# Kernel optimization log

Hardware: AMD Instinct MI355X
Metric: run time of the kernel (lower is better)

## Reference

```python
import jax, jax.numpy as jnp
import numpy as np

N = 8192        # nodes
E = 262144      # edges (avg degree 32)
D = 128         # input_dim
H = 128         # hidden_dim
O = 64          # output_dim (classes)
C = 4096        # codebook_size
LAMB_EDGE = 1.0
LAMB_NODE = 1.0
COMMIT_W = 0.25


def l2norm(x):
    return x / jnp.clip(jnp.linalg.norm(x, axis=-1, keepdims=True), 1e-12)


def graph_conv(x, W, b, src, dst, n):
    # DGL GraphConv, norm='both': D_out^{-1/2} on src, sum-aggregate, D_in^{-1/2} on dst, then xW+b, relu
    ones = jnp.ones(src.shape[0], x.dtype)
    deg_out = jax.ops.segment_sum(ones, src, num_segments=n)
    deg_in = jax.ops.segment_sum(ones, dst, num_segments=n)
    norm_src = jnp.where(deg_out > 0, jax.lax.rsqrt(jnp.maximum(deg_out, 1e-12)), 0.0)
    norm_dst = jnp.where(deg_in > 0, jax.lax.rsqrt(jnp.maximum(deg_in, 1e-12)), 0.0)
    h = x * norm_src[:, None]
    m = jax.ops.segment_sum(h[src], dst, num_segments=n)  # message passing (irregular gather/scatter)
    h = m * norm_dst[:, None]
    return jax.nn.relu(h @ W + b)


def setup_inputs() -> dict:
    key = jax.random.key(0)
    ks = jax.random.split(key, 16)
    feats = jax.random.normal(ks[0], (N, D), jnp.float32)
    src = jax.random.randint(ks[1], (E,), 0, N)
    dst = jax.random.randint(ks[2], (E,), 0, N)
    s = 1.0 / np.sqrt(D)
    sh = 1.0 / np.sqrt(H)
    return {
        'feats': feats, 'src': src, 'dst': dst,
        'W1': jax.random.normal(ks[3], (D, D), jnp.float32) * s,
        'b1': jnp.zeros((D,), jnp.float32),
        'W2': jax.random.normal(ks[4], (D, H), jnp.float32) * s,
        'b2': jnp.zeros((H,), jnp.float32),
        'dec1_W': jax.random.normal(ks[5], (D, D), jnp.float32) * s,
        'dec1_b': jnp.zeros((D,), jnp.float32),
        'dec2_W': jax.random.normal(ks[6], (D, D), jnp.float32) * s,
        'dec2_b': jnp.zeros((D,), jnp.float32),
        'lin_W': jax.random.normal(ks[7], (H, O), jnp.float32) * sh,
        'lin_b': jnp.zeros((O,), jnp.float32),
        'codebook': jax.random.normal(ks[8], (C, D), jnp.float32),
    }


def reference(feats, src, dst, W1, b1, W2, b2, dec1_W, dec1_b, dec2_W, dec2_b, lin_W, lin_b, codebook):
    n = feats.shape[0]
    # layer 1: GraphConv(D -> D)
    h1 = graph_conv(feats, W1, b1, src, dst, n)  # [N, D]

    # VectorQuantize with cosine similarity codebook
    xn = l2norm(h1)
    cn = l2norm(codebook)                 # [C, D]
    dist = xn @ cn.T                      # [N, C] cosine similarity
    ind = jnp.argmax(dist, axis=-1)       # [N]
    q = cn[ind]                           # [N, D] nearest (normalized) codes
    commit_loss = COMMIT_W * jnp.mean((jax.lax.stop_gradient(q) - h1) ** 2)
    quantized = h1 + jax.lax.stop_gradient(q - h1)  # straight-through

    quantized_edge = quantized @ dec1_W + dec1_b
    quantized_node = quantized @ dec2_W + dec2_b
    feature_rec_loss = LAMB_NODE * jnp.mean((h1 - quantized_node) ** 2)

    # dense adjacency reconstruction
    adj = jnp.zeros((n, n), feats.dtype).at[src, dst].set(1.0)
    adj_q = quantized_edge @ quantized_edge.T          # [N, N]
    adj_q = (adj_q - adj_q.min()) / (adj_q.max() - adj_q.min())
    edge_rec_loss = LAMB_EDGE * jnp.sqrt(jnp.mean((adj - adj_q) ** 2))

    # layer 2: GraphConv(D -> H) on quantized_edge, then linear head
    h3 = graph_conv(quantized_edge, W2, b2, src, dst, n)
    out = h3 @ lin_W + lin_b                           # [N, O]

    loss = feature_rec_loss + edge_rec_loss + commit_loss
    h_list = (h1, quantized, h3)
    return (h_list, out, loss, dist, cn)
```

## Files before the change

kernel.cpp:

```cpp
#include <hip/hip_runtime.h>
#include <cstdint>

constexpr int N = 8192, E = 262144, D = 128, O = 64, C = 4096;

#define DEV __device__ __forceinline__

typedef short s8v __attribute__((ext_vector_type(8)));
typedef float f4v __attribute__((ext_vector_type(4)));

DEV unsigned fmap(float f) {
  unsigned u = __float_as_uint(f);
  return (u & 0x80000000u) ? ~u : (u | 0x80000000u);
}
DEV float funmap(unsigned u) {
  unsigned o = (u & 0x80000000u) ? (u & 0x7FFFFFFFu) : ~u;
  return __uint_as_float(o);
}
DEV unsigned short f2bf(float f) {
  uint32_t b = __float_as_uint(f);
  return (unsigned short)((b + 0x7FFFu + ((b >> 16) & 1u)) >> 16);
}
DEV float bf2f(unsigned short h) { return __uint_as_float((uint32_t)h << 16); }


__global__ __launch_bounds__(256) void k_degree(const int* __restrict__ src, const int* __restrict__ dst,
    uint32_t* __restrict__ bits, int* __restrict__ dego, int* __restrict__ degi,
    uint32_t* __restrict__ scal_u) {
  int e = blockIdx.x * 256 + threadIdx.x;
  int s = src[e], d = dst[e];
  atomicAdd(&dego[s], 1);
  atomicAdd(&degi[d], 1);
  unsigned idx = (unsigned)s * 8192u + (unsigned)d;
  unsigned bit = 1u << (idx & 31);
  unsigned old = atomicOr(&bits[idx >> 5], bit);
  bool isnew = !(old & bit);
  unsigned long long b = __ballot(isnew);
  if ((threadIdx.x & 63) == 0) atomicAdd(&scal_u[2], (unsigned)__popcll(b));
}

__global__ __launch_bounds__(256) void k_norms(const int* __restrict__ dego, const int* __restrict__ degi,
                                               float* __restrict__ nsrc, float* __restrict__ ndst) {
  int i = blockIdx.x * 256 + threadIdx.x;
  if (i >= N) return;
  int a = dego[i], b = degi[i];
  nsrc[i] = a > 0 ? 1.0f / sqrtf((float)a) : 0.0f;
  ndst[i] = b > 0 ? 1.0f / sqrtf((float)b) : 0.0f;
}

__global__ __launch_bounds__(1024) void k_scan(const int* __restrict__ degi, int* __restrict__ rowptr,
                                               int* __restrict__ cursor) {
  __shared__ int sh[1024];
  int tid = threadIdx.x;
  int base = tid * 8;
  int v[8];
  int s = 0;
#pragma unroll
  for (int j = 0; j < 8; ++j) { v[j] = degi[base + j]; s += v[j]; }
  sh[tid] = s;
  __syncthreads();
  for (int off = 1; off < 1024; off <<= 1) {
    int t = (tid >= off) ? sh[tid - off] : 0;
    __syncthreads();
    sh[tid] += t;
    __syncthreads();
  }
  int run = (tid == 0) ? 0 : sh[tid - 1];
#pragma unroll
  for (int j = 0; j < 8; ++j) { rowptr[base + j] = run; cursor[base + j] = run; run += v[j]; }
  if (tid == 1023) rowptr[N] = run;
}

__global__ __launch_bounds__(256) void k_scatter(const int* __restrict__ src, const int* __restrict__ dst,
                                                 int* __restrict__ cursor, int* __restrict__ csr) {
  int e = blockIdx.x * 256 + threadIdx.x;
  int d = dst[e];
  int pos = atomicAdd(&cursor[d], 1);
  csr[pos] = src[e];
}

__global__ __launch_bounds__(256) void k_scale(const float4* __restrict__ in, const float* __restrict__ norm,
                                               float4* __restrict__ out) {
  int i = blockIdx.x * 256 + threadIdx.x;
  if (i >= N * 32) return;
  float s = norm[i >> 5];
  float4 v = in[i];
  v.x *= s; v.y *= s; v.z *= s; v.w *= s;
  out[i] = v;
}

__global__ __launch_bounds__(256) void k_tobf16(const float4* __restrict__ in, ushort4* __restrict__ out) {
  int i = blockIdx.x * 256 + threadIdx.x;
  if (i >= N * 32) return;
  float4 v = in[i];
  ushort4 o;
  o.x = f2bf(v.x); o.y = f2bf(v.y); o.z = f2bf(v.z); o.w = f2bf(v.w);
  out[i] = o;
}

__global__ __launch_bounds__(256) void k_split(const float4* __restrict__ in,
    ushort4* __restrict__ hi, ushort4* __restrict__ lo, int n4) {
  int i = blockIdx.x * 256 + threadIdx.x;
  if (i >= n4) return;
  float4 v = in[i];
  ushort4 h, l;
  h.x = f2bf(v.x); h.y = f2bf(v.y); h.z = f2bf(v.z); h.w = f2bf(v.w);
  l.x = f2bf(v.x - bf2f(h.x)); l.y = f2bf(v.y - bf2f(h.y));
  l.z = f2bf(v.z - bf2f(h.z)); l.w = f2bf(v.w - bf2f(h.w));
  hi[i] = h; lo[i] = l;
}

__global__ __launch_bounds__(128) void k_aggregate(const int* __restrict__ rowptr, const int* __restrict__ csr,
    const float* __restrict__ tmp, const float* __restrict__ ndst, float* __restrict__ out) {
  int row = blockIdx.x, t = threadIdx.x;
  int e0 = rowptr[row], e1 = rowptr[row + 1];
  float acc = 0.f;
  int e = e0;
  for (; e + 4 <= e1; e += 4) {
    int s0 = csr[e], s1 = csr[e + 1], s2 = csr[e + 2], s3 = csr[e + 3];
    acc += tmp[s0 * 128 + t];
    acc += tmp[s1 * 128 + t];
    acc += tmp[s2 * 128 + t];
    acc += tmp[s3 * 128 + t];
  }
  for (; e < e1; ++e) acc += tmp[csr[e] * 128 + t];
  out[row * 128 + t] = acc * ndst[row];
}

__global__ __launch_bounds__(256) void k_l2norm(const float* __restrict__ in, float* __restrict__ out_al,
                                                float* __restrict__ out_extra, int rows) {
  int wave = threadIdx.x >> 6, lane = threadIdx.x & 63;
  int row = blockIdx.x * 4 + wave;
  if (row >= rows) return;
  float2 v = ((const float2*)in)[row * 64 + lane];
  float ss = v.x * v.x + v.y * v.y;
#pragma unroll
  for (int o = 32; o > 0; o >>= 1) ss += __shfl_xor(ss, o);
  float den = fmaxf(sqrtf(ss), 1e-12f);
  float ox = v.x / den, oy = v.y / den;
  ((float2*)out_al)[row * 64 + lane] = make_float2(ox, oy);
  if (out_extra != nullptr) {
    out_extra[row * 128 + 2 * lane] = ox;
    out_extra[row * 128 + 2 * lane + 1] = oy;
  }
}

template <int CO, bool RELU>
__global__ __launch_bounds__(256, 2) void k_mm(const float* __restrict__ A, const float* __restrict__ W,
    const float* __restrict__ bias, float* __restrict__ out) {
  constexpr int CG = CO / 4;
  constexpr int RG = 256 / CG;
  constexpr int TR = RG * 4;
  constexpr int WIT = (64 * CG) / 256;
  __shared__ __align__(16) float Al[TR * 128];
  __shared__ __align__(16) float Wl[64 * CO];
  int tid = threadIdx.x;
  int cg = tid % CG, rg = tid / CG;
  int rbase = blockIdx.x * TR;
#pragma unroll
  for (int it = 0; it < TR / 8; ++it) {
    int idx = tid + it * 256;
    int r = idx >> 5, c = idx & 31;
    *(float4*)&Al[r * 128 + c * 4] = *(const float4*)&A[(rbase + r) * 128 + c * 4];
  }
  float acc[4][4] = {};
  for (int kc = 0; kc < 128; kc += 64) {
    __syncthreads();
#pragma unroll
    for (int it = 0; it < WIT; ++it) {
      int idx = tid + it * 256;
      int r = idx / CG, c = idx % CG;
      *(float4*)&Wl[r * CO + c * 4] = *(const float4*)&W[(kc + r) * CO + c * 4];
    }
    __syncthreads();
#pragma unroll
    for (int k = 0; k < 64; ++k) {
      float4 w4 = *(const float4*)&Wl[k * CO + cg * 4];
#pragma unroll
      for (int i = 0; i < 4; ++i) {
        float a = Al[(rg * 4 + i) * 128 + kc + k];
        acc[i][0] += a * w4.x; acc[i][1] += a * w4.y; acc[i][2] += a * w4.z; acc[i][3] += a * w4.w;
      }
    }
  }
  float4 b4 = *(const float4*)&bias[cg * 4];
#pragma unroll
  for (int i = 0; i < 4; ++i) {
    float4 o;
    o.x = acc[i][0] + b4.x; o.y = acc[i][1] + b4.y; o.z = acc[i][2] + b4.z; o.w = acc[i][3] + b4.w;
    if (RELU) { o.x = fmaxf(o.x, 0.f); o.y = fmaxf(o.y, 0.f); o.z = fmaxf(o.z, 0.f); o.w = fmaxf(o.w, 0.f); }
    *(float4*)&out[(rbase + rg * 4 + i) * CO + cg * 4] = o;
  }
}

__global__ __launch_bounds__(256) void k_dist(
    const unsigned short* __restrict__ xhi, const unsigned short* __restrict__ xlo,
    const unsigned short* __restrict__ chi, const unsigned short* __restrict__ clo,
    float* __restrict__ dout, unsigned long long* __restrict__ pbk, float* __restrict__ pbv2) {
  int bx = blockIdx.x, by = blockIdx.y;
  int rbase = by * 128, cbase = bx * 128;
  __shared__ __align__(16) unsigned short As[128 * 132];
  __shared__ __align__(16) unsigned short Bs[128 * 132];
  int tid = threadIdx.x;
  int wave = tid >> 6, lane = tid & 63;
  int l15 = lane & 15, quad = lane >> 4;
  int wr = wave * 32;

#pragma unroll
  for (int it = 0; it < 8; ++it) {
    int idx = tid + it * 256;
    int r = idx >> 4, ch = idx & 15;
    *(s8v*)&As[r * 132 + ch * 8] = *(const s8v*)&xhi[(rbase + r) * 128 + ch * 8];
    *(s8v*)&Bs[r * 132 + ch * 8] = *(const s8v*)&chi[(cbase + r) * 128 + ch * 8];
  }
  __syncthreads();
  s8v ah[2][4], al[2][4];
#pragma unroll
  for (int rt = 0; rt < 2; ++rt)
#pragma unroll
    for (int kq = 0; kq < 4; ++kq)
      ah[rt][kq] = *(const s8v*)&As[(wr + rt * 16 + l15) * 132 + kq * 32 + quad * 8];
  __syncthreads();
#pragma unroll
  for (int it = 0; it < 8; ++it) {
    int idx = tid + it * 256;
    int r = idx >> 4, ch = idx & 15;
    *(s8v*)&As[r * 132 + ch * 8] = *(const s8v*)&xlo[(rbase + r) * 128 + ch * 8];
  }
  __syncthreads();
#pragma unroll
  for (int rt = 0; rt < 2; ++rt)
#pragma unroll
    for (int kq = 0; kq < 4; ++kq)
      al[rt][kq] = *(const s8v*)&As[(wr + rt * 16 + l15) * 132 + kq * 32 + quad * 8];

  f4v acc[2][8];
#pragma unroll
  for (int rt = 0; rt < 2; ++rt)
#pragma unroll
    for (int ct = 0; ct < 8; ++ct) acc[rt][ct] = {0.f, 0.f, 0.f, 0.f};

#pragma unroll
  for (int ct = 0; ct < 8; ++ct) {
    s8v b[4];
#pragma unroll
    for (int kq = 0; kq < 4; ++kq)
      b[kq] = *(const s8v*)&Bs[(ct * 16 + l15) * 132 + kq * 32 + quad * 8];
#pragma unroll
    for (int rt = 0; rt < 2; ++rt)
#pragma unroll
      for (int kq = 0; kq < 4; ++kq) {
        acc[rt][ct] = __builtin_amdgcn_mfma_f32_16x16x32_bf16(ah[rt][kq], b[kq], acc[rt][ct], 0, 0, 0);
        acc[rt][ct] = __builtin_amdgcn_mfma_f32_16x16x32_bf16(al[rt][kq], b[kq], acc[rt][ct], 0, 0, 0);
      }
  }
  __syncthreads();
#pragma unroll
  for (int it = 0; it < 8; ++it) {
    int idx = tid + it * 256;
    int r = idx >> 4, ch = idx & 15;
    *(s8v*)&Bs[r * 132 + ch * 8] = *(const s8v*)&clo[(cbase + r) * 128 + ch * 8];
  }
  __syncthreads();
#pragma unroll
  for (int ct = 0; ct < 8; ++ct) {
    s8v b[4];
#pragma unroll
    for (int kq = 0; kq < 4; ++kq)
      b[kq] = *(const s8v*)&Bs[(ct * 16 + l15) * 132 + kq * 32 + quad * 8];
#pragma unroll
    for (int rt = 0; rt < 2; ++rt)
#pragma unroll
      for (int kq = 0; kq < 4; ++kq)
        acc[rt][ct] = __builtin_amdgcn_mfma_f32_16x16x32_bf16(ah[rt][kq], b[kq], acc[rt][ct], 0, 0, 0);
  }

  float b1v[2][4], b2v[2][4];
  unsigned c1v[2][4];
#pragma unroll
  for (int rt = 0; rt < 2; ++rt)
#pragma unroll
    for (int reg = 0; reg < 4; ++reg) { b1v[rt][reg] = -3.4e38f; b2v[rt][reg] = -3.4e38f; c1v[rt][reg] = 0; }
#pragma unroll
  for (int rt = 0; rt < 2; ++rt)
#pragma unroll
    for (int ct = 0; ct < 8; ++ct)
#pragma unroll
      for (int reg = 0; reg < 4; ++reg) {
        float v = acc[rt][ct][reg];
        int row = rbase + wr + rt * 16 + quad * 4 + reg;
        int col = cbase + ct * 16 + l15;
        dout[(size_t)row * 4096 + col] = v;
        if (v > b1v[rt][reg]) { b2v[rt][reg] = b1v[rt][reg]; b1v[rt][reg] = v; c1v[rt][reg] = (unsigned)col; }
        else if (v > b2v[rt][reg]) b2v[rt][reg] = v;
      }
  __syncthreads();
  unsigned long long* sck = (unsigned long long*)As;
  float* scv = (float*)Bs;
#pragma unroll
  for (int rt = 0; rt < 2; ++rt)
#pragma unroll
    for (int reg = 0; reg < 4; ++reg) {
      int rloc = wr + rt * 16 + quad * 4 + reg;
      sck[rloc * 16 + l15] =
          (((unsigned long long)fmap(b1v[rt][reg])) << 32) |
          (unsigned long long)(0xFFFFFFFFu - c1v[rt][reg]);
      scv[rloc * 16 + l15] = b2v[rt][reg];
    }
  __syncthreads();
  if (tid < 128) {
    unsigned long long m = 0ull;
#pragma unroll
    for (int l = 0; l < 16; ++l) {
      unsigned long long t = sck[tid * 16 + l];
      m = t > m ? t : m;
    }
    float v2 = -3.4e38f;
#pragma unroll
    for (int l = 0; l < 16; ++l) {
      unsigned long long k = sck[tid * 16 + l];
      float c = (k == m) ? scv[tid * 16 + l] : funmap((unsigned)(k >> 32));
      v2 = fmaxf(v2, c);
    }
    pbk[(size_t)(rbase + tid) * 32 + bx] = m;
    pbv2[(size_t)(rbase + tid) * 32 + bx] = v2;
  }
}

__global__ __launch_bounds__(128) void k_q(const unsigned long long* __restrict__ pbk,
    const float* __restrict__ pbv2, const float* __restrict__ xn, const float* __restrict__ cnws,
    const float* __restrict__ h1, float* __restrict__ qout, float* __restrict__ pq) {
  int row = blockIdx.x, t = threadIdx.x;
  int e = t & 31;
  unsigned long long k = pbk[(size_t)row * 32 + e];
  float v2l = pbv2[(size_t)row * 32 + e];
  unsigned long long m = k;
#pragma unroll
  for (int o = 32; o > 0; o >>= 1) {
    unsigned long long s = __shfl_xor(m, o);
    m = s > m ? s : m;
  }
  float cand = (k == m) ? v2l : funmap((unsigned)(k >> 32));
#pragma unroll
  for (int o = 32; o > 0; o >>= 1) cand = fmaxf(cand, __shfl_xor(cand, o));
  float gap = funmap((unsigned)(m >> 32)) - cand;
  int col;
  __shared__ float xr[128];
  __shared__ unsigned long long bw[2];
  if (gap < 2e-4f) {
    xr[t] = xn[row * 128 + t];
    __syncthreads();
    unsigned long long best = 0ull;
    for (int i = 0; i < 32; ++i) {
      int c = t + i * 128;
      const float* cp = &cnws[c * 128];
      float s = 0.f;
#pragma unroll 8
      for (int kk = 0; kk < 128; ++kk) s += xr[kk] * cp[kk];
      unsigned long long key = (((unsigned long long)fmap(s)) << 32) |
                               (unsigned long long)(0xFFFFFFFFu - (unsigned)c);
      if (key > best) best = key;
    }
#pragma unroll
    for (int o = 32; o > 0; o >>= 1) {
      unsigned long long s2 = __shfl_xor(best, o);
      best = s2 > best ? s2 : best;
    }
    if ((t & 63) == 0) bw[t >> 6] = best;
    __syncthreads();
    best = bw[0] > bw[1] ? bw[0] : bw[1];
    col = (int)(0xFFFFFFFFu - (unsigned)(best & 0xFFFFFFFFull));
  } else {
    col = (int)(0xFFFFFFFFu - (unsigned)(m & 0xFFFFFFFFull));
  }
  float q = cnws[col * 128 + t];
  qout[row * 128 + t] = q;
  float dd = q - h1[row * 128 + t];
  float ss = dd * dd;
#pragma unroll
  for (int o = 32; o > 0; o >>= 1) ss += __shfl_xor(ss, o);
  __shared__ float p[2];
  if ((t & 63) == 0) p[t >> 6] = ss;
  __syncthreads();
  if (t == 0) pq[row] = p[0] + p[1];
}

__global__ __launch_bounds__(256) void k_adjq(const unsigned short* __restrict__ qb,
    const uint32_t* __restrict__ bits,
    double* __restrict__ p_sum, double* __restrict__ p_sq, double* __restrict__ p_es,
    float* __restrict__ p_mn, float* __restrict__ p_mx) {
  int bx = blockIdx.x, by = blockIdx.y;
  int pid = by * gridDim.x + bx;
  int tid = threadIdx.x;
  if (bx < by) {
    if (tid == 0) {
      p_sum[pid] = 0.0; p_sq[pid] = 0.0; p_es[pid] = 0.0;
      p_mn[pid] = 3.4e38f; p_mx[pid] = -3.4e38f;
    }
    return;
  }
  int rbase = by * 128, cbase = bx * 128;
  __shared__ unsigned short Ab[128 * 132];
  __shared__ unsigned short Bb[128 * 132];
#pragma unroll
  for (int it = 0; it < 8; ++it) {
    int idx = tid + it * 256;
    int r = idx >> 4, ch = idx & 15;
    *(s8v*)&Ab[r * 132 + ch * 8] = *(const s8v*)&qb[(rbase + r) * 128 + ch * 8];
    *(s8v*)&Bb[r * 132 + ch * 8] = *(const s8v*)&qb[(cbase + r) * 128 + ch * 8];
  }
  __syncthreads();
  int wave = tid >> 6, lane = tid & 63;
  int l15 = lane & 15, quad = lane >> 4;
  int wr = wave * 32;
  f4v acc[2][8];
#pragma unroll
  for (int rt = 0; rt < 2; ++rt)
#pragma unroll
    for (int ct = 0; ct < 8; ++ct) acc[rt][ct] = {0.f, 0.f, 0.f, 0.f};
  s8v a[2][4];
#pragma unroll
  for (int rt = 0; rt < 2; ++rt)
#pragma unroll
    for (int kq = 0; kq < 4; ++kq)
      a[rt][kq] = *(const s8v*)&Ab[(wr + rt * 16 + l15) * 132 + kq * 32 + quad * 8];
#pragma unroll
  for (int ct = 0; ct < 8; ++ct) {
    s8v b[4];
#pragma unroll
    for (int kq = 0; kq < 4; ++kq)
      b[kq] = *(const s8v*)&Bb[(ct * 16 + l15) * 132 + kq * 32 + quad * 8];
#pragma unroll
    for (int rt = 0; rt < 2; ++rt)
#pragma unroll
      for (int kq = 0; kq < 4; ++kq)
        acc[rt][ct] = __builtin_amdgcn_mfma_f32_16x16x32_bf16(a[rt][kq], b[kq], acc[rt][ct], 0, 0, 0);
  }
  __syncthreads();
  uint32_t* bl = (uint32_t*)Ab;
  uint32_t* blT = bl + 512;
#pragma unroll
  for (int it = 0; it < 2; ++it) {
    int idx = tid + it * 256;
    int r = idx >> 2, wq = idx & 3;
    bl[idx] = bits[(rbase + r) * 256 + (cbase >> 5) + wq];
    blT[idx] = bits[(cbase + r) * 256 + (rbase >> 5) + wq];
  }
  __syncthreads();
  float lsum = 0.f, lsq = 0.f, les = 0.f;
  float lmin = 3.4e38f, lmax = -3.4e38f;
  bool diag = (bx == by);
#pragma unroll
  for (int rt = 0; rt < 2; ++rt)
#pragma unroll
    for (int ct = 0; ct < 8; ++ct)
#pragma unroll
      for (int reg = 0; reg < 4; ++reg) {
        int lr = wr + rt * 16 + quad * 4 + reg;
        int lc = ct * 16 + l15;
        if (diag && lc < lr) continue;
        float v = acc[rt][ct][reg];
        bool ondiag = diag && (lc == lr);
        float wgt = ondiag ? 1.f : 2.f;
        lsum += wgt * v;
        lsq += wgt * v * v;
        lmin = fminf(lmin, v);
        lmax = fmaxf(lmax, v);
        unsigned eb = (bl[lr * 4 + (lc >> 5)] >> (lc & 31)) & 1u;
        if (!ondiag) eb += (blT[lc * 4 + (lr >> 5)] >> (lr & 31)) & 1u;
        if (eb) les += (float)eb * v;
      }
  double dsum = (double)lsum, dsq = (double)lsq, des = (double)les;
#pragma unroll
  for (int o = 32; o > 0; o >>= 1) {
    dsum += __shfl_xor(dsum, o);
    dsq += __shfl_xor(dsq, o);
    des += __shfl_xor(des, o);
    lmin = fminf(lmin, __shfl_xor(lmin, o));
    lmax = fmaxf(lmax, __shfl_xor(lmax, o));
  }
  double* shd = (double*)Bb;
  float* shf = (float*)(shd + 12);
  if (lane == 0) {
    shd[wave * 3 + 0] = dsum; shd[wave * 3 + 1] = dsq; shd[wave * 3 + 2] = des;
    shf[wave * 2 + 0] = lmin; shf[wave * 2 + 1] = lmax;
  }
  __syncthreads();
  if (tid == 0) {
    double s = 0.0, q = 0.0, e = 0.0;
    float m0 = 3.4e38f, m1 = -3.4e38f;
#pragma unroll
    for (int w0 = 0; w0 < 4; ++w0) {
      s += shd[w0 * 3 + 0]; q += shd[w0 * 3 + 1]; e += shd[w0 * 3 + 2];
      m0 = fminf(m0, shf[w0 * 2 + 0]); m1 = fmaxf(m1, shf[w0 * 2 + 1]);
    }
    p_sum[pid] = s; p_sq[pid] = q; p_es[pid] = e;
    p_mn[pid] = m0; p_mx[pid] = m1;
  }
}

__global__ __launch_bounds__(256) void k_sqdiff(const float4* __restrict__ a, const float4* __restrict__ b,
                                                float* __restrict__ ps) {
  int i = blockIdx.x * 256 + threadIdx.x;
  float s = 0.f;
  const int total = N * 32;
  for (; i < total; i += gridDim.x * 256) {
    float4 x = a[i], y = b[i];
    float d0 = x.x - y.x, d1 = x.y - y.y, d2 = x.z - y.z, d3 = x.w - y.w;
    s += d0 * d0 + d1 * d1 + d2 * d2 + d3 * d3;
  }
#pragma unroll
  for (int o = 32; o > 0; o >>= 1) s += __shfl_xor(s, o);
  __shared__ float p[4];
  if ((threadIdx.x & 63) == 0) p[threadIdx.x >> 6] = s;
  __syncthreads();
  if (threadIdx.x == 0) ps[blockIdx.x] = p[0] + p[1] + p[2] + p[3];
}

__global__ __launch_bounds__(1024) void k_finish(const double* __restrict__ p_sum,
    const double* __restrict__ p_sq, const double* __restrict__ p_es,
    const float* __restrict__ p_mn, const float* __restrict__ p_mx,
    const float* __restrict__ pq, const float* __restrict__ ps,
    const uint32_t* __restrict__ scal_u, float* __restrict__ o_loss) {
  int tid = threadIdx.x;
  double sum = 0.0, sq = 0.0, es = 0.0, commit = 0.0, frec = 0.0;
  float mn = 3.4e38f, mx = -3.4e38f;
  for (int i = tid; i < 4096; i += 1024) {
    sum += p_sum[i]; sq += p_sq[i]; es += p_es[i];
    mn = fminf(mn, p_mn[i]); mx = fmaxf(mx, p_mx[i]);
  }
  for (int i = tid; i < 8192; i += 1024) commit += (double)pq[i];
  if (tid < 512) frec = (double)ps[tid];
#pragma unroll
  for (int o = 32; o > 0; o >>= 1) {
    sum += __shfl_xor(sum, o); sq += __shfl_xor(sq, o); es += __shfl_xor(es, o);
    commit += __shfl_xor(commit, o); frec += __shfl_xor(frec, o);
    mn = fminf(mn, __shfl_xor(mn, o)); mx = fmaxf(mx, __shfl_xor(mx, o));
  }
  __shared__ double shd[16][5];
  __shared__ float shf[16][2];
  int wave = tid >> 6, lane = tid & 63;
  if (lane == 0) {
    shd[wave][0] = sum; shd[wave][1] = sq; shd[wave][2] = es;
    shd[wave][3] = commit; shd[wave][4] = frec;
    shf[wave][0] = mn; shf[wave][1] = mx;
  }
  __syncthreads();
  if (tid == 0) {
    double s = 0, q = 0, e = 0, c = 0, f = 0;
    float m0 = 3.4e38f, m1 = -3.4e38f;
    for (int w0 = 0; w0 < 16; ++w0) {
      s += shd[w0][0]; q += shd[w0][1]; e += shd[w0][2]; c += shd[w0][3]; f += shd[w0][4];
      m0 = fminf(m0, shf[w0][0]); m1 = fmaxf(m1, shf[w0][1]);
    }
    double mnd = (double)m0, mxd = (double)m1, U = (double)scal_u[2];
    const double N2 = 67108864.0;
    double scl = 1.0 / (mxd - mnd);
    double mean = (scl * scl * (q - 2.0 * mnd * s + mnd * mnd * N2) - 2.0 * scl * (e - mnd * U) + U) / N2;
    *o_loss = (float)(f / 1048576.0 + sqrt(mean) + 0.25 * c / 1048576.0);
  }
}

extern "C" void kernel_launch(void* const* d_in, const int* in_sizes, int n_in,
                              void* d_out, int out_size, void* d_ws, size_t ws_size,
                              hipStream_t stream) {
  (void)in_sizes; (void)n_in; (void)out_size;
  const float* feats = (const float*)d_in[0];
  const int* src = (const int*)d_in[1];
  const int* dst = (const int*)d_in[2];
  const float* W1 = (const float*)d_in[3];
  const float* b1 = (const float*)d_in[4];
  const float* W2 = (const float*)d_in[5];
  const float* b2 = (const float*)d_in[6];
  const float* dec1W = (const float*)d_in[7];
  const float* dec1b = (const float*)d_in[8];
  const float* dec2W = (const float*)d_in[9];
  const float* dec2b = (const float*)d_in[10];
  const float* linW = (const float*)d_in[11];
  const float* linb = (const float*)d_in[12];
  const float* codebook = (const float*)d_in[13];

  float* out = (float*)d_out;
  float* o_h1 = out;
  float* o_q = out + 1048576;
  float* o_h3 = out + 2097152;
  float* o_out = out + 3145728;
  float* o_loss = out + 3670016;
  float* o_dist = out + 3670017;
  float* o_cn = out + 37224449;

  char* w = (char*)d_ws;
  size_t off = 0;
  auto alloc = [&](size_t b) { char* p = w + off; off = (off + b + 255) & ~(size_t)255; return p; };
  uint32_t* bits = (uint32_t*)alloc(8388608);
  int* dego = (int*)alloc(N * 4);
  int* degi = (int*)alloc(N * 4);
  uint32_t* scal_u = (uint32_t*)alloc(256);
  size_t zero_bytes = off;
  int* rowptr = (int*)alloc((N + 1) * 4);
  int* cursor = (int*)alloc(N * 4);
  int* csr = (int*)alloc(E * 4);
  float* nsrc = (float*)alloc(N * 4);
  float* ndst = (float*)alloc(N * 4);
  float* tmp = (float*)alloc((size_t)N * D * 4);
  float* agg = (float*)alloc((size_t)N * D * 4);
  float* xn = (float*)alloc((size_t)N * D * 4);
  float* cnws = (float*)alloc((size_t)C * D * 4);
  float* qe = (float*)alloc((size_t)N * D * 4);
  float* qn = (float*)alloc((size_t)N * D * 4);
  double* p_sum = (double*)alloc(4096 * 8);
  double* p_sq = (double*)alloc(4096 * 8);
  double* p_es = (double*)alloc(4096 * 8);
  float* p_mn = (float*)alloc(4096 * 4);
  float* p_mx = (float*)alloc(4096 * 4);
  float* pq = (float*)alloc(8192 * 4);
  float* ps = (float*)alloc(512 * 4);
  unsigned short* qb = (unsigned short*)tmp;
  unsigned short* xhi = (unsigned short*)qe;
  unsigned short* xlo = (unsigned short*)(qe + 524288);
  unsigned short* chi = (unsigned short*)qn;
  unsigned short* clo = (unsigned short*)(qn + 262144);
  unsigned long long* pbk = (unsigned long long*)agg;
  float* pbv2 = (float*)(agg + 524288);
  if (ws_size < off) return;

  hipMemsetAsync(d_ws, 0, zero_bytes, stream);

  k_degree<<<E / 256, 256, 0, stream>>>(src, dst, bits, dego, degi, scal_u);
  k_norms<<<N / 256, 256, 0, stream>>>(dego, degi, nsrc, ndst);
  k_scan<<<1, 1024, 0, stream>>>(degi, rowptr, cursor);
  k_scatter<<<E / 256, 256, 0, stream>>>(src, dst, cursor, csr);

  k_scale<<<N * 32 / 256, 256, 0, stream>>>((const float4*)feats, nsrc, (float4*)tmp);
  k_aggregate<<<N, 128, 0, stream>>>(rowptr, csr, tmp, ndst, agg);
  k_mm<128, true><<<N / 32, 256, 0, stream>>>(agg, W1, b1, o_h1);

  k_l2norm<<<C / 4, 256, 0, stream>>>(codebook, cnws, o_cn, C);
  k_l2norm<<<N / 4, 256, 0, stream>>>(o_h1, xn, nullptr, N);
  k_split<<<N * 32 / 256, 256, 0, stream>>>((const float4*)xn, (ushort4*)xhi, (ushort4*)xlo, N * 32);
  k_split<<<C * 32 / 256, 256, 0, stream>>>((const float4*)cnws, (ushort4*)chi, (ushort4*)clo, C * 32);
  k_dist<<<dim3(C / 128, N / 128), 256, 0, stream>>>(xhi, xlo, chi, clo, o_dist, pbk, pbv2);
  k_q<<<N, 128, 0, stream>>>(pbk, pbv2, xn, cnws, o_h1, o_q, pq);

  k_mm<128, false><<<N / 32, 256, 0, stream>>>(o_q, dec1W, dec1b, qe);
  k_mm<128, false><<<N / 32, 256, 0, stream>>>(o_q, dec2W, dec2b, qn);
  k_sqdiff<<<512, 256, 0, stream>>>((const float4*)o_h1, (const float4*)qn, ps);

  k_tobf16<<<N * 32 / 256, 256, 0, stream>>>((const float4*)qe, (ushort4*)qb);
  k_adjq<<<dim3(N / 128, N / 128), 256, 0, stream>>>(qb, bits, p_sum, p_sq, p_es, p_mn, p_mx);

  k_scale<<<N * 32 / 256, 256, 0, stream>>>((const float4*)qe, nsrc, (float4*)tmp);
  k_aggregate<<<N, 128, 0, stream>>>(rowptr, csr, tmp, ndst, agg);
  k_mm<128, true><<<N / 32, 256, 0, stream>>>(agg, W2, b2, o_h3);
  k_mm<64, false><<<N / 64, 256, 0, stream>>>(o_h3, linW, linb, o_out);

  k_finish<<<1, 1024, 0, stream>>>(p_sum, p_sq, p_es, p_mn, p_mx, pq, ps, scal_u, o_loss);
}
```

Baseline: 606.4 us.

## Defer near-tie argmax recomputation to a compacted fix-up kernel over a transposed codebook

The per-row quantize kernel no longer performs the exact fp32 rescan of all 4096 codes inside divergent blocks when the top-two gap is small. Instead it appends those rows to a flagged list through an atomic counter. A separate kernel then rescans only the flagged rows with 256 threads, reading a transposed codebook so the loads coalesce. This removes a long-tail stall from the N-block kernel, but adds a transpose kernel and an extra launch, and relies on scal_u[3] being zeroed by the memset.

```diff
diff --git a/kernel.cpp b/kernel.cpp
--- a/kernel.cpp
+++ b/kernel.cpp
@@ -109,6 +109,25 @@
   hi[i] = h; lo[i] = l;
 }
 
+__global__ __launch_bounds__(256) void k_transpose(const float* __restrict__ in, float* __restrict__ outT) {
+  __shared__ float tl[64][133];
+  int t = threadIdx.x;
+  int cbase = blockIdx.x * 64;
+#pragma unroll
+  for (int it = 0; it < 32; ++it) {
+    int idx = t + it * 256;
+    int r = idx >> 7, k = idx & 127;
+    tl[r][k] = in[(cbase + r) * 128 + k];
+  }
+  __syncthreads();
+#pragma unroll
+  for (int it = 0; it < 32; ++it) {
+    int idx = t + it * 256;
+    int k = idx >> 6, c = idx & 63;
+    outT[k * 4096 + cbase + c] = tl[c][k];
+  }
+}
+
 __global__ __launch_bounds__(128) void k_aggregate(const int* __restrict__ rowptr, const int* __restrict__ csr,
     const float* __restrict__ tmp, const float* __restrict__ ndst, float* __restrict__ out) {
   int row = blockIdx.x, t = threadIdx.x;
@@ -327,8 +346,9 @@
 }
 
 __global__ __launch_bounds__(128) void k_q(const unsigned long long* __restrict__ pbk,
-    const float* __restrict__ pbv2, const float* __restrict__ xn, const float* __restrict__ cnws,
-    const float* __restrict__ h1, float* __restrict__ qout, float* __restrict__ pq) {
+    const float* __restrict__ pbv2, const float* __restrict__ cnws,
+    const float* __restrict__ h1, float* __restrict__ qout, float* __restrict__ pq,
+    uint32_t* __restrict__ scal_u, int* __restrict__ flagged) {
   int row = blockIdx.x, t = threadIdx.x;
   int e = t & 31;
   unsigned long long k = pbk[(size_t)row * 32 + e];
@@ -343,35 +363,11 @@
 #pragma unroll
   for (int o = 32; o > 0; o >>= 1) cand = fmaxf(cand, __shfl_xor(cand, o));
   float gap = funmap((unsigned)(m >> 32)) - cand;
-  int col;
-  __shared__ float xr[128];
-  __shared__ unsigned long long bw[2];
-  if (gap < 2e-4f) {
-    xr[t] = xn[row * 128 + t];
-    __syncthreads();
-    unsigned long long best = 0ull;
-    for (int i = 0; i < 32; ++i) {
-      int c = t + i * 128;
-      const float* cp = &cnws[c * 128];
-      float s = 0.f;
-#pragma unroll 8
-      for (int kk = 0; kk < 128; ++kk) s += xr[kk] * cp[kk];
-      unsigned long long key = (((unsigned long long)fmap(s)) << 32) |
-                               (unsigned long long)(0xFFFFFFFFu - (unsigned)c);
-      if (key > best) best = key;
-    }
-#pragma unroll
-    for (int o = 32; o > 0; o >>= 1) {
-      unsigned long long s2 = __shfl_xor(best, o);
-      best = s2 > best ? s2 : best;
-    }
-    if ((t & 63) == 0) bw[t >> 6] = best;
-    __syncthreads();
-    best = bw[0] > bw[1] ? bw[0] : bw[1];
-    col = (int)(0xFFFFFFFFu - (unsigned)(best & 0xFFFFFFFFull));
-  } else {
-    col = (int)(0xFFFFFFFFu - (unsigned)(m & 0xFFFFFFFFull));
-  }
+  if (gap < 2e-4f && t == 0) {
+    unsigned idx = atomicAdd(&scal_u[3], 1u);
+    flagged[idx] = row;
+  }
+  int col = (int)(0xFFFFFFFFu - (unsigned)(m & 0xFFFFFFFFull));
   float q = cnws[col * 128 + t];
   qout[row * 128 + t] = q;
   float dd = q - h1[row * 128 + t];
@@ -382,6 +378,62 @@
   if ((t & 63) == 0) p[t >> 6] = ss;
   __syncthreads();
   if (t == 0) pq[row] = p[0] + p[1];
+}
+
+__global__ __launch_bounds__(256) void k_fix(const uint32_t* __restrict__ scal_u,
+    const int* __restrict__ flagged, const float* __restrict__ xn,
+    const float* __restrict__ cnwsT, const float* __restrict__ cnws,
+    const float* __restrict__ h1, float* __restrict__ qout, float* __restrict__ pq) {
+  int nf = (int)scal_u[3];
+  int t = threadIdx.x;
+  __shared__ float xr[128];
+  __shared__ unsigned long long bw4[4];
+  __shared__ float pp[2];
+  for (int i = blockIdx.x; i < nf; i += gridDim.x) {
+    int row = flagged[i];
+    __syncthreads();
+    if (t < 128) xr[t] = xn[row * 128 + t];
+    __syncthreads();
+    float s[16];
+#pragma unroll
+    for (int j = 0; j < 16; ++j) s[j] = 0.f;
+    for (int k = 0; k < 128; ++k) {
+      float xv = xr[k];
+      const float* cp = &cnwsT[k * 4096 + t];
+#pragma unroll
+      for (int j = 0; j < 16; ++j) s[j] = fmaf(xv, cp[j * 256], s[j]);
+    }
+    unsigned long long best = 0ull;
+#pragma unroll
+    for (int j = 0; j < 16; ++j) {
+      unsigned c = (unsigned)(j * 256 + t);
+      unsigned long long key = (((unsigned long long)fmap(s[j])) << 32) |
+                               (unsigned long long)(0xFFFFFFFFu - c);
+      if (key > best) best = key;
+    }
+#pragma unroll
+    for (int o = 32; o > 0; o >>= 1) {
+      unsigned long long s2 = __shfl_xor(best, o);
+      best = s2 > best ? s2 : best;
+    }
+    if ((t & 63) == 0) bw4[t >> 6] = best;
+    __syncthreads();
+    unsigned long long b0 = bw4[0] > bw4[1] ? bw4[0] : bw4[1];
+    unsigned long long b1 = bw4[2] > bw4[3] ? bw4[2] : bw4[3];
+    best = b0 > b1 ? b0 : b1;
+    int col = (int)(0xFFFFFFFFu - (unsigned)(best & 0xFFFFFFFFull));
+    if (t < 128) {
+      float q = cnws[col * 128 + t];
+      qout[(size_t)row * 128 + t] = q;
+      float dd = q - h1[row * 128 + t];
+      float ss = dd * dd;
+#pragma unroll
+      for (int o = 32; o > 0; o >>= 1) ss += __shfl_xor(ss, o);
+      if ((t & 63) == 0) pp[t >> 6] = ss;
+    }
+    __syncthreads();
+    if (t == 0) pq[row] = pp[0] + pp[1];
+  }
 }
 
 __global__ __launch_bounds__(256) void k_adjq(const unsigned short* __restrict__ qb,
@@ -614,7 +666,9 @@
   float* p_mx = (float*)alloc(4096 * 4);
   float* pq = (float*)alloc(8192 * 4);
   float* ps = (float*)alloc(512 * 4);
+  int* flagged = (int*)alloc(8192 * 4);
   unsigned short* qb = (unsigned short*)tmp;
+  float* cnwsT = tmp;
   unsigned short* xhi = (unsigned short*)qe;
   unsigned short* xlo = (unsigned short*)(qe + 524288);
   unsigned short* chi = (unsigned short*)qn;
@@ -636,10 +690,12 @@
 
   k_l2norm<<<C / 4, 256, 0, stream>>>(codebook, cnws, o_cn, C);
   k_l2norm<<<N / 4, 256, 0, stream>>>(o_h1, xn, nullptr, N);
+  k_transpose<<<C / 64, 256, 0, stream>>>(cnws, cnwsT);
   k_split<<<N * 32 / 256, 256, 0, stream>>>((const float4*)xn, (ushort4*)xhi, (ushort4*)xlo, N * 32);
   k_split<<<C * 32 / 256, 256, 0, stream>>>((const float4*)cnws, (ushort4*)chi, (ushort4*)clo, C * 32);
   k_dist<<<dim3(C / 128, N / 128), 256, 0, stream>>>(xhi, xlo, chi, clo, o_dist, pbk, pbv2);
-  k_q<<<N, 128, 0, stream>>>(pbk, pbv2, xn, cnws, o_h1, o_q, pq);
+  k_q<<<N, 128, 0, stream>>>(pbk, pbv2, cnws, o_h1, o_q, pq, scal_u, flagged);
+  k_fix<<<128, 256, 0, stream>>>(scal_u, flagged, xn, cnwsT, cnws, o_h1, o_q, pq);
 
   k_mm<128, false><<<N / 32, 256, 0, stream>>>(o_q, dec1W, dec1b, qe);
   k_mm<128, false><<<N / 32, 256, 0, stream>>>(o_q, dec2W, dec2b, qn);
```

Measured after the change: 526.7 us. -13.1%, faster.
